# Performance work log

Measured on AMD Instinct MI355X. Metric: run time of the kernel, lower is better.

Reference implementation:

```python
import jax, jax.numpy as jnp
import numpy as np

N_NODES = 100000
N_EDGES = 1250000
D = 64
N_LAYERS = 4


def setup_inputs() -> dict:
    key = jax.random.key(0)
    ks = jax.random.split(key, 6)
    x = jax.random.normal(ks[0], (N_NODES, D), dtype=jnp.float32)
    edge_index = jax.random.randint(ks[1], (2, N_EDGES), 0, N_NODES, dtype=jnp.int64)
    s = 1.0 / np.sqrt(D)
    # PyG SAGEConv per layer: lin_l (applied to aggregated neighbors, with bias)
    # and lin_r (applied to self features, no bias). All layers are 64->64, so stack.
    Wl = jax.random.uniform(ks[2], (N_LAYERS, D, D), dtype=jnp.float32, minval=-s, maxval=s)
    bl = jax.random.uniform(ks[3], (N_LAYERS, D), dtype=jnp.float32, minval=-s, maxval=s)
    Wr = jax.random.uniform(ks[4], (N_LAYERS, D, D), dtype=jnp.float32, minval=-s, maxval=s)
    return {"x": x, "edge_index": edge_index, "Wl": Wl, "bl": bl, "Wr": Wr}


def reference(x, edge_index, Wl, bl, Wr):
    src = edge_index[0]  # message source: x_j
    dst = edge_index[1]  # aggregate at target node
    h = x
    for i in range(N_LAYERS):
        msg = h[src]  # [E, D] irregular gather
        agg = jax.ops.segment_max(msg, dst, num_segments=N_NODES)  # max-pool aggregation
        agg = jnp.where(jnp.isneginf(agg), 0.0, agg)  # empty segments -> 0 (PyG convention)
        h = jax.nn.relu(agg @ Wl[i] + bl[i] + h @ Wr[i])
    return h
```

## Files before the change

kernel.cpp:

```cpp
#include <hip/hip_runtime.h>
#include <hip/hip_fp16.h>
#include <stdint.h>

#define NN 100000
#define NE 1250000
#define DD 64
#define NL 4

#define NPART3 256
#define PSIZE3 391
#define TILE4 1024
#define NTB ((NE / 4 + TILE4 - 1) / TILE4)
#define SCANA_N (NPART3 * NTB)
#define SRCBITS 17

#define MB2 64
#define L2BLOCKS ((NN + MB2 - 1) / MB2)
#define APAD 136
#define CPADH 72
#define CPADF 68

typedef _Float16 half8 __attribute__((ext_vector_type(8)));
typedef _Float16 half2v __attribute__((ext_vector_type(2)));
typedef float floatx4 __attribute__((ext_vector_type(4)));
typedef int intx4 __attribute__((ext_vector_type(4)));

__device__ __forceinline__ unsigned f2h2(float a, float b) {
    __half2 h = __floats2half2_rn(a, b);
    return *reinterpret_cast<unsigned*>(&h);
}
__device__ __forceinline__ unsigned umax2(unsigned a, unsigned b) {
    half2v x = *reinterpret_cast<half2v*>(&a);
    half2v y = *reinterpret_cast<half2v*>(&b);
    half2v r = __builtin_elementwise_max(x, y);
    return *reinterpret_cast<unsigned*>(&r);
}

__global__ __launch_bounds__(256) void cast_kernel(const float* __restrict__ x,
                                                   __half* __restrict__ hh) {
    int i = blockIdx.x * 256 + threadIdx.x;
    float4 v = ((const float4*)x)[i];
    uint2 u;
    u.x = f2h2(v.x, v.y);
    u.y = f2h2(v.z, v.w);
    ((uint2*)hh)[i] = u;
}

__global__ __launch_bounds__(256) void countA_kernel(const int* __restrict__ dst,
                                                     int* __restrict__ blockcnt) {
    __shared__ int cnt[NPART3];
    int tid = threadIdx.x;
    cnt[tid] = 0;
    __syncthreads();
    int b = blockIdx.x;
    #pragma unroll
    for (int r = 0; r < 4; ++r) {
        int i4 = b * TILE4 + r * 256 + tid;
        if (i4 < NE / 4) {
            intx4 d = __builtin_nontemporal_load(&((const intx4*)dst)[i4]);
            atomicAdd(&cnt[(unsigned)d.x / PSIZE3], 1);
            atomicAdd(&cnt[(unsigned)d.y / PSIZE3], 1);
            atomicAdd(&cnt[(unsigned)d.z / PSIZE3], 1);
            atomicAdd(&cnt[(unsigned)d.w / PSIZE3], 1);
        }
    }
    __syncthreads();
    blockcnt[tid * NTB + b] = cnt[tid];
}

__global__ __launch_bounds__(512) void scanP1_kernel(int* __restrict__ blockcnt,
                                                     int* __restrict__ rowsum) {
    __shared__ int sm[512];
    int p = blockIdx.x;
    int tid = threadIdx.x;
    int v = (tid < NTB) ? blockcnt[p * NTB + tid] : 0;
    sm[tid] = v;
    __syncthreads();
    for (int off = 1; off < 512; off <<= 1) {
        int t = (tid >= off) ? sm[tid - off] : 0;
        __syncthreads();
        sm[tid] += t;
        __syncthreads();
    }
    if (tid < NTB) blockcnt[p * NTB + tid] = sm[tid] - v;
    if (tid == 511) rowsum[p] = sm[511];
}

__global__ __launch_bounds__(256) void scanP2_kernel(int* __restrict__ rowsum) {
    __shared__ int sm[256];
    int tid = threadIdx.x;
    int v = rowsum[tid];
    sm[tid] = v;
    __syncthreads();
    for (int off = 1; off < 256; off <<= 1) {
        int t = (tid >= off) ? sm[tid - off] : 0;
        __syncthreads();
        sm[tid] += t;
        __syncthreads();
    }
    rowsum[tid] = sm[tid] - v;
}

__global__ __launch_bounds__(256) void scatterA_kernel(const int* __restrict__ src,
                                                       const int* __restrict__ dst,
                                                       const int* __restrict__ blockcnt,
                                                       const int* __restrict__ rowoff,
                                                       int* __restrict__ ebufP) {
    __shared__ int cur[NPART3];
    int tid = threadIdx.x;
    int b = blockIdx.x;
    cur[tid] = rowoff[tid] + blockcnt[tid * NTB + b];
    __syncthreads();
    #pragma unroll
    for (int r = 0; r < 4; ++r) {
        int i4 = b * TILE4 + r * 256 + tid;
        if (i4 < NE / 4) {
            intx4 d = __builtin_nontemporal_load(&((const intx4*)dst)[i4]);
            intx4 s = __builtin_nontemporal_load(&((const intx4*)src)[i4]);
            int part, p;
            part = (unsigned)d.x / PSIZE3; p = atomicAdd(&cur[part], 1);
            ebufP[p] = ((d.x - part * PSIZE3) << SRCBITS) | s.x;
            part = (unsigned)d.y / PSIZE3; p = atomicAdd(&cur[part], 1);
            ebufP[p] = ((d.y - part * PSIZE3) << SRCBITS) | s.y;
            part = (unsigned)d.z / PSIZE3; p = atomicAdd(&cur[part], 1);
            ebufP[p] = ((d.z - part * PSIZE3) << SRCBITS) | s.z;
            part = (unsigned)d.w / PSIZE3; p = atomicAdd(&cur[part], 1);
            ebufP[p] = ((d.w - part * PSIZE3) << SRCBITS) | s.w;
        }
    }
}

__global__ __launch_bounds__(1024) void fillD_kernel(const int* __restrict__ ebufP,
                                                     const int* __restrict__ rowoff,
                                                     int* __restrict__ row_start,
                                                     int* __restrict__ csr) {
    __shared__ int cnt[PSIZE3];
    __shared__ int localstart[PSIZE3];
    __shared__ int partial[1024];
    int part = blockIdx.x;
    int tid = threadIdx.x;
    int nbase = part * PSIZE3;
    int base = rowoff[part];
    int hi = (part < NPART3 - 1) ? rowoff[part + 1] : NE;

    if (tid < PSIZE3) cnt[tid] = 0;
    __syncthreads();

    for (int i = base + tid; i < hi; i += 1024)
        atomicAdd(&cnt[(unsigned)ebufP[i] >> SRCBITS], 1);
    __syncthreads();

    int e0 = (tid < PSIZE3) ? cnt[tid] : 0;
    int s = e0;
    partial[tid] = s;
    __syncthreads();
    for (int off = 1; off < 1024; off <<= 1) {
        int v = (tid >= off) ? partial[tid - off] : 0;
        __syncthreads();
        partial[tid] += v;
        __syncthreads();
    }
    int run = partial[tid] - s;
    if (tid < PSIZE3) localstart[tid] = run;
    __syncthreads();

    int nmax = NN - nbase; if (nmax > PSIZE3) nmax = PSIZE3;
    if (tid < nmax) row_start[nbase + tid] = base + localstart[tid];
    if (part == NPART3 - 1 && tid == 0) row_start[NN] = NE;

    if (tid < PSIZE3) cnt[tid] = 0;
    __syncthreads();

    for (int i = base + tid; i < hi; i += 1024) {
        int p = ebufP[i];
        int dl = (unsigned)p >> SRCBITS;
        int local = atomicAdd(&cnt[dl], 1);
        csr[base + localstart[dl] + local] = p & ((1 << SRCBITS) - 1);
    }
}

__global__ __launch_bounds__(256) void agg_kernel(const __half* __restrict__ hh,
                                                  const int* __restrict__ row_start,
                                                  const int* __restrict__ csr,
                                                  __half* __restrict__ aggh) {
    int tid = threadIdx.x;
    int wv = tid >> 6;
    int lane = tid & 63;
    int g = lane >> 3;
    int c8 = (lane & 7) * 8;
    int n0 = blockIdx.x * 8 + wv * 2;
    int n1 = n0 + 1;
    int base0 = row_start[n0];
    int base1 = row_start[n1];
    int cnt0 = base1 - base0;
    int cnt1 = row_start[n1 + 1] - base1;
    int cl0 = cnt0 - 1;
    int cl1 = cnt1 - 1;

    int idx0 = 0, idx1 = 0;
    if (cnt0 > 0) idx0 = csr[base0 + ((lane <= cl0) ? lane : cl0)];
    if (cnt1 > 0) idx1 = csr[base1 + ((lane <= cl1) ? lane : cl1)];

    const uint4 NI4 = make_uint4(0xFC00FC00u, 0xFC00FC00u, 0xFC00FC00u, 0xFC00FC00u);
    uint4 acc0 = (cnt0 > 0) ? NI4 : make_uint4(0, 0, 0, 0);
    uint4 acc1 = (cnt1 > 0) ? NI4 : make_uint4(0, 0, 0, 0);

    int m0 = (cnt0 < 64) ? cnt0 : 64;
    int m1 = (cnt1 < 64) ? cnt1 : 64;
    int kmax = (m0 > m1) ? m0 : m1;

    for (int k = 0; k < kmax; k += 16) {
        int ka = k + g;
        int kb = k + g + 8;
        int s00 = 0, s01 = 0, s10 = 0, s11 = 0;
        if (cnt0 > 0) {
            s00 = __shfl(idx0, (ka <= cl0) ? ka : cl0, 64);
            s01 = __shfl(idx0, (kb <= cl0) ? kb : cl0, 64);
        }
        if (cnt1 > 0) {
            s10 = __shfl(idx1, (ka <= cl1) ? ka : cl1, 64);
            s11 = __shfl(idx1, (kb <= cl1) ? kb : cl1, 64);
        }
        if (ka < m0) {
            uint4 u = *(const uint4*)&hh[(size_t)s00 * DD + c8];
            acc0.x = umax2(acc0.x, u.x); acc0.y = umax2(acc0.y, u.y);
            acc0.z = umax2(acc0.z, u.z); acc0.w = umax2(acc0.w, u.w);
        }
        if (ka < m1) {
            uint4 u = *(const uint4*)&hh[(size_t)s10 * DD + c8];
            acc1.x = umax2(acc1.x, u.x); acc1.y = umax2(acc1.y, u.y);
            acc1.z = umax2(acc1.z, u.z); acc1.w = umax2(acc1.w, u.w);
        }
        if (kb < m0) {
            uint4 u = *(const uint4*)&hh[(size_t)s01 * DD + c8];
            acc0.x = umax2(acc0.x, u.x); acc0.y = umax2(acc0.y, u.y);
            acc0.z = umax2(acc0.z, u.z); acc0.w = umax2(acc0.w, u.w);
        }
        if (kb < m1) {
            uint4 u = *(const uint4*)&hh[(size_t)s11 * DD + c8];
            acc1.x = umax2(acc1.x, u.x); acc1.y = umax2(acc1.y, u.y);
            acc1.z = umax2(acc1.z, u.z); acc1.w = umax2(acc1.w, u.w);
        }
    }
    for (int k = 64 + g; k < cnt0; k += 8) {
        int s = csr[base0 + k];
        uint4 u = *(const uint4*)&hh[(size_t)s * DD + c8];
        acc0.x = umax2(acc0.x, u.x); acc0.y = umax2(acc0.y, u.y);
        acc0.z = umax2(acc0.z, u.z); acc0.w = umax2(acc0.w, u.w);
    }
    for (int k = 64 + g; k < cnt1; k += 8) {
        int s = csr[base1 + k];
        uint4 u = *(const uint4*)&hh[(size_t)s * DD + c8];
        acc1.x = umax2(acc1.x, u.x); acc1.y = umax2(acc1.y, u.y);
        acc1.z = umax2(acc1.z, u.z); acc1.w = umax2(acc1.w, u.w);
    }

    #pragma unroll
    for (int off = 8; off <= 32; off <<= 1) {
        acc0.x = umax2(acc0.x, (unsigned)__shfl_xor((int)acc0.x, off, 64));
        acc0.y = umax2(acc0.y, (unsigned)__shfl_xor((int)acc0.y, off, 64));
        acc0.z = umax2(acc0.z, (unsigned)__shfl_xor((int)acc0.z, off, 64));
        acc0.w = umax2(acc0.w, (unsigned)__shfl_xor((int)acc0.w, off, 64));
        acc1.x = umax2(acc1.x, (unsigned)__shfl_xor((int)acc1.x, off, 64));
        acc1.y = umax2(acc1.y, (unsigned)__shfl_xor((int)acc1.y, off, 64));
        acc1.z = umax2(acc1.z, (unsigned)__shfl_xor((int)acc1.z, off, 64));
        acc1.w = umax2(acc1.w, (unsigned)__shfl_xor((int)acc1.w, off, 64));
    }
    if (lane < 8) {
        *(uint4*)&aggh[(size_t)n0 * DD + c8] = acc0;
        *(uint4*)&aggh[(size_t)n1 * DD + c8] = acc1;
    }
}

__global__ __launch_bounds__(256, 4) void layer_mfma_kernel(
        const __half* __restrict__ aggh,
        __half* __restrict__ hh,
        float* __restrict__ hout,
        const float* __restrict__ Wl,
        const float* __restrict__ bl,
        const float* __restrict__ Wr,
        int last) {
    __shared__ char smem[2 * MB2 * APAD * 2];
    _Float16* a_s  = (_Float16*)smem;
    _Float16* bt_s = (_Float16*)(smem + MB2 * APAD * 2);

    int tid = threadIdx.x;
    int lane = tid & 63;
    int w = tid >> 6;
    int node0 = blockIdx.x * MB2;

    #pragma unroll
    for (int i = 0; i < 4; ++i) {
        int idx = i * 256 + tid;
        int r = idx >> 4;
        int c4 = idx & 15;
        int node = node0 + r; if (node > NN - 1) node = NN - 1;
        const __half* srcp = (c4 < 8) ? (aggh + (size_t)node * DD + c4 * 8)
                                      : (hh + (size_t)node * DD + (c4 - 8) * 8);
        uint4 v = *(const uint4*)srcp;
        *(uint4*)&a_s[r * APAD + c4 * 8] = v;
    }
    {
        int n = tid & 63;
        int kb = tid >> 6;
        #pragma unroll
        for (int kk = 0; kk < 32; ++kk) {
            int k = kb * 32 + kk;
            float wv = (k < 64) ? Wl[k * DD + n] : Wr[(k - 64) * DD + n];
            bt_s[n * APAD + k] = (_Float16)wv;
        }
    }
    __syncthreads();

    floatx4 acc[4];
    #pragma unroll
    for (int nt = 0; nt < 4; ++nt) acc[nt] = (floatx4){0.f, 0.f, 0.f, 0.f};
    int m = lane & 15;
    int q = lane >> 4;

    #pragma unroll
    for (int ks = 0; ks < 4; ++ks) {
        half8 af = *(half8*)&a_s[(w * 16 + m) * APAD + q * 8 + ks * 32];
        #pragma unroll
        for (int nt = 0; nt < 4; ++nt) {
            half8 bf = *(half8*)&bt_s[(nt * 16 + m) * APAD + q * 8 + ks * 32];
            acc[nt] = __builtin_amdgcn_mfma_f32_16x16x32_f16(af, bf, acc[nt], 0, 0, 0);
        }
    }
    __syncthreads();

    _Float16* ch = (_Float16*)smem;
    float*    cf = (float*)(smem + MB2 * CPADH * 2);

    #pragma unroll
    for (int nt = 0; nt < 4; ++nt) {
        int col = nt * 16 + m;
        float b = bl[col];
        #pragma unroll
        for (int r = 0; r < 4; ++r) {
            int rowl = w * 16 + q * 4 + r;
            float o = fmaxf(acc[nt][r] + b, 0.0f);
            if (last) cf[rowl * CPADF + col] = o;
            else      ch[rowl * CPADH + col] = (_Float16)o;
        }
    }
    __syncthreads();

    if (!last) {
        #pragma unroll
        for (int i = 0; i < 2; ++i) {
            int idx = i * 256 + tid;
            int r = idx >> 3;
            int c4 = idx & 7;
            int node = node0 + r;
            if (node < NN) {
                uint4 v = *(uint4*)&ch[r * CPADH + c4 * 8];
                *(uint4*)&hh[(size_t)node * DD + c4 * 8] = v;
            }
        }
    } else {
        #pragma unroll
        for (int i = 0; i < 4; ++i) {
            int idx = i * 256 + tid;
            int r = idx >> 4;
            int c4 = idx & 15;
            int node = node0 + r;
            if (node < NN) {
                float4 v = *(float4*)&cf[r * CPADF + c4 * 4];
                *(float4*)&hout[(size_t)node * DD + c4 * 4] = v;
            }
        }
    }
}

extern "C" void kernel_launch(void* const* d_in, const int* in_sizes, int n_in,
                              void* d_out, int out_size, void* d_ws, size_t ws_size,
                              hipStream_t stream) {
    const float* x  = (const float*)d_in[0];
    const int*   ei = (const int*)d_in[1];
    const float* Wl = (const float*)d_in[2];
    const float* bl = (const float*)d_in[3];
    const float* Wr = (const float*)d_in[4];
    float* h = (float*)d_out;

    const int* src = ei;
    const int* dst = ei + NE;

    char* ws = (char*)d_ws;
    __half* aggh     = (__half*)ws;  ws += (size_t)NN * DD * sizeof(__half);
    __half* hh       = (__half*)ws;  ws += (size_t)NN * DD * sizeof(__half);
    int* row_start   = (int*)ws;     ws += (size_t)(NN + 16) * sizeof(int);
    int* blockcnt    = (int*)ws;     ws += (size_t)(SCANA_N + 16) * sizeof(int);
    int* rowsum      = (int*)ws;     ws += (size_t)(NPART3 + 16) * sizeof(int);
    int* csr         = (int*)ws;

    int* ebufP = (int*)aggh;

    cast_kernel<<<(NN * DD / 4) / 256, 256, 0, stream>>>(x, hh);

    countA_kernel<<<NTB, 256, 0, stream>>>(dst, blockcnt);
    scanP1_kernel<<<NPART3, 512, 0, stream>>>(blockcnt, rowsum);
    scanP2_kernel<<<1, 256, 0, stream>>>(rowsum);
    scatterA_kernel<<<NTB, 256, 0, stream>>>(src, dst, blockcnt, rowsum, ebufP);
    fillD_kernel<<<NPART3, 1024, 0, stream>>>(ebufP, rowsum, row_start, csr);

    for (int l = 0; l < NL; ++l) {
        agg_kernel<<<NN / 8, 256, 0, stream>>>(hh, row_start, csr, aggh);
        layer_mfma_kernel<<<L2BLOCKS, 256, 0, stream>>>(
            aggh, hh, h, Wl + (size_t)l * DD * DD, bl + (size_t)l * DD, Wr + (size_t)l * DD * DD,
            (l == NL - 1) ? 1 : 0);
    }
}
```

Before: 282.4 us.

## Split feature table into four column slabs for cache-local gather aggregation

Stores the fp16 node features and aggregates as four column slabs of 16 halves each (slab-major), and runs the max-aggregation with a 2D grid where blockIdx.y selects the slab. Each slab is 3.2 MB, so a pass over one slab's random gathers is meant to stay resident in L2/LLC instead of thrashing the full 12.8 MB table. The agg kernel now handles 4 nodes per wave with 16 lanes each, and uses nontemporal loads for the CSR. In exchange the CSR and row_start are read four times, and the cast and MFMA kernels take strided slab addressing.

```diff
diff --git a/kernel.cpp b/kernel.cpp
--- a/kernel.cpp
+++ b/kernel.cpp
@@ -37,13 +37,18 @@
 }
 
 __global__ __launch_bounds__(256) void cast_kernel(const float* __restrict__ x,
-                                                   __half* __restrict__ hh) {
+                                                   __half* __restrict__ hh4) {
     int i = blockIdx.x * 256 + threadIdx.x;
     float4 v = ((const float4*)x)[i];
     uint2 u;
     u.x = f2h2(v.x, v.y);
     u.y = f2h2(v.z, v.w);
-    ((uint2*)hh)[i] = u;
+    int j = i * 4;
+    int n = j >> 6;
+    int col = j & 63;
+    int s = col >> 4;
+    int c = col & 15;
+    ((uint2*)hh4)[((size_t)s * NN + n) * 4 + (c >> 2)] = u;
 }
 
 __global__ __launch_bounds__(256) void countA_kernel(const int* __restrict__ dst,
@@ -179,102 +184,68 @@
     }
 }
 
-__global__ __launch_bounds__(256) void agg_kernel(const __half* __restrict__ hh,
+__global__ __launch_bounds__(256) void agg_kernel(const __half* __restrict__ hh4,
                                                   const int* __restrict__ row_start,
                                                   const int* __restrict__ csr,
-                                                  __half* __restrict__ aggh) {
+                                                  __half* __restrict__ agg4) {
     int tid = threadIdx.x;
     int wv = tid >> 6;
     int lane = tid & 63;
-    int g = lane >> 3;
-    int c8 = (lane & 7) * 8;
-    int n0 = blockIdx.x * 8 + wv * 2;
-    int n1 = n0 + 1;
-    int base0 = row_start[n0];
-    int base1 = row_start[n1];
-    int cnt0 = base1 - base0;
-    int cnt1 = row_start[n1 + 1] - base1;
-    int cl0 = cnt0 - 1;
-    int cl1 = cnt1 - 1;
-
-    int idx0 = 0, idx1 = 0;
-    if (cnt0 > 0) idx0 = csr[base0 + ((lane <= cl0) ? lane : cl0)];
-    if (cnt1 > 0) idx1 = csr[base1 + ((lane <= cl1) ? lane : cl1)];
+    int nq = lane >> 4;
+    int l16 = lane & 15;
+    int sl = l16 >> 1;
+    int sub = lane & 1;
+    int s = blockIdx.y;
+    int n = blockIdx.x * 16 + wv * 4 + nq;
+
+    int base = row_start[n];
+    int cnt  = row_start[n + 1] - base;
+    int cl = cnt - 1;
+
+    int idx16 = 0;
+    if (cnt > 0) idx16 = __builtin_nontemporal_load(&csr[base + ((l16 <= cl) ? l16 : cl)]);
+
+    const __half* tab = hh4 + (size_t)s * NN * 16;
 
     const uint4 NI4 = make_uint4(0xFC00FC00u, 0xFC00FC00u, 0xFC00FC00u, 0xFC00FC00u);
-    uint4 acc0 = (cnt0 > 0) ? NI4 : make_uint4(0, 0, 0, 0);
-    uint4 acc1 = (cnt1 > 0) ? NI4 : make_uint4(0, 0, 0, 0);
-
-    int m0 = (cnt0 < 64) ? cnt0 : 64;
-    int m1 = (cnt1 < 64) ? cnt1 : 64;
-    int kmax = (m0 > m1) ? m0 : m1;
-
-    for (int k = 0; k < kmax; k += 16) {
-        int ka = k + g;
-        int kb = k + g + 8;
-        int s00 = 0, s01 = 0, s10 = 0, s11 = 0;
-        if (cnt0 > 0) {
-            s00 = __shfl(idx0, (ka <= cl0) ? ka : cl0, 64);
-            s01 = __shfl(idx0, (kb <= cl0) ? kb : cl0, 64);
-        }
-        if (cnt1 > 0) {
-            s10 = __shfl(idx1, (ka <= cl1) ? ka : cl1, 64);
-            s11 = __shfl(idx1, (kb <= cl1) ? kb : cl1, 64);
-        }
-        if (ka < m0) {
-            uint4 u = *(const uint4*)&hh[(size_t)s00 * DD + c8];
-            acc0.x = umax2(acc0.x, u.x); acc0.y = umax2(acc0.y, u.y);
-            acc0.z = umax2(acc0.z, u.z); acc0.w = umax2(acc0.w, u.w);
-        }
-        if (ka < m1) {
-            uint4 u = *(const uint4*)&hh[(size_t)s10 * DD + c8];
-            acc1.x = umax2(acc1.x, u.x); acc1.y = umax2(acc1.y, u.y);
-            acc1.z = umax2(acc1.z, u.z); acc1.w = umax2(acc1.w, u.w);
-        }
-        if (kb < m0) {
-            uint4 u = *(const uint4*)&hh[(size_t)s01 * DD + c8];
-            acc0.x = umax2(acc0.x, u.x); acc0.y = umax2(acc0.y, u.y);
-            acc0.z = umax2(acc0.z, u.z); acc0.w = umax2(acc0.w, u.w);
-        }
-        if (kb < m1) {
-            uint4 u = *(const uint4*)&hh[(size_t)s11 * DD + c8];
-            acc1.x = umax2(acc1.x, u.x); acc1.y = umax2(acc1.y, u.y);
-            acc1.z = umax2(acc1.z, u.z); acc1.w = umax2(acc1.w, u.w);
-        }
-    }
-    for (int k = 64 + g; k < cnt0; k += 8) {
-        int s = csr[base0 + k];
-        uint4 u = *(const uint4*)&hh[(size_t)s * DD + c8];
-        acc0.x = umax2(acc0.x, u.x); acc0.y = umax2(acc0.y, u.y);
-        acc0.z = umax2(acc0.z, u.z); acc0.w = umax2(acc0.w, u.w);
-    }
-    for (int k = 64 + g; k < cnt1; k += 8) {
-        int s = csr[base1 + k];
-        uint4 u = *(const uint4*)&hh[(size_t)s * DD + c8];
-        acc1.x = umax2(acc1.x, u.x); acc1.y = umax2(acc1.y, u.y);
-        acc1.z = umax2(acc1.z, u.z); acc1.w = umax2(acc1.w, u.w);
-    }
-
-    #pragma unroll
-    for (int off = 8; off <= 32; off <<= 1) {
-        acc0.x = umax2(acc0.x, (unsigned)__shfl_xor((int)acc0.x, off, 64));
-        acc0.y = umax2(acc0.y, (unsigned)__shfl_xor((int)acc0.y, off, 64));
-        acc0.z = umax2(acc0.z, (unsigned)__shfl_xor((int)acc0.z, off, 64));
-        acc0.w = umax2(acc0.w, (unsigned)__shfl_xor((int)acc0.w, off, 64));
-        acc1.x = umax2(acc1.x, (unsigned)__shfl_xor((int)acc1.x, off, 64));
-        acc1.y = umax2(acc1.y, (unsigned)__shfl_xor((int)acc1.y, off, 64));
-        acc1.z = umax2(acc1.z, (unsigned)__shfl_xor((int)acc1.z, off, 64));
-        acc1.w = umax2(acc1.w, (unsigned)__shfl_xor((int)acc1.w, off, 64));
-    }
-    if (lane < 8) {
-        *(uint4*)&aggh[(size_t)n0 * DD + c8] = acc0;
-        *(uint4*)&aggh[(size_t)n1 * DD + c8] = acc1;
+    uint4 acc = (cnt > 0) ? NI4 : make_uint4(0, 0, 0, 0);
+
+    int km = cnt;
+    km = max(km, __shfl_xor(km, 16, 64));
+    km = max(km, __shfl_xor(km, 32, 64));
+
+    for (int k = 0; k < km; k += 8) {
+        int ka = k + sl;
+        int srcv;
+        if (k < 16) {
+            int cka = (ka <= cl) ? ka : cl;
+            if (cka < 0) cka = 0;
+            srcv = __shfl(idx16, (nq << 4) + cka, 64);
+        } else {
+            srcv = (ka < cnt) ? __builtin_nontemporal_load(&csr[base + ka]) : 0;
+        }
+        if (ka < cnt) {
+            uint4 u = *(const uint4*)&tab[(size_t)srcv * 16 + sub * 8];
+            acc.x = umax2(acc.x, u.x); acc.y = umax2(acc.y, u.y);
+            acc.z = umax2(acc.z, u.z); acc.w = umax2(acc.w, u.w);
+        }
+    }
+
+    #pragma unroll
+    for (int off = 2; off <= 8; off <<= 1) {
+        acc.x = umax2(acc.x, (unsigned)__shfl_xor((int)acc.x, off, 64));
+        acc.y = umax2(acc.y, (unsigned)__shfl_xor((int)acc.y, off, 64));
+        acc.z = umax2(acc.z, (unsigned)__shfl_xor((int)acc.z, off, 64));
+        acc.w = umax2(acc.w, (unsigned)__shfl_xor((int)acc.w, off, 64));
+    }
+    if (l16 < 2) {
+        *(uint4*)&agg4[((size_t)s * NN + n) * 16 + sub * 8] = acc;
     }
 }
 
 __global__ __launch_bounds__(256, 4) void layer_mfma_kernel(
-        const __half* __restrict__ aggh,
-        __half* __restrict__ hh,
+        const __half* __restrict__ agg4,
+        __half* __restrict__ hh4,
         float* __restrict__ hout,
         const float* __restrict__ Wl,
         const float* __restrict__ bl,
@@ -295,8 +266,12 @@
         int r = idx >> 4;
         int c4 = idx & 15;
         int node = node0 + r; if (node > NN - 1) node = NN - 1;
-        const __half* srcp = (c4 < 8) ? (aggh + (size_t)node * DD + c4 * 8)
-                                      : (hh + (size_t)node * DD + (c4 - 8) * 8);
+        const __half* srcp;
+        if (c4 < 8) srcp = agg4 + ((size_t)(c4 >> 1) * NN + node) * 16 + (c4 & 1) * 8;
+        else {
+            int cc = c4 - 8;
+            srcp = hh4 + ((size_t)(cc >> 1) * NN + node) * 16 + (cc & 1) * 8;
+        }
         uint4 v = *(const uint4*)srcp;
         *(uint4*)&a_s[r * APAD + c4 * 8] = v;
     }
@@ -355,7 +330,7 @@
             int node = node0 + r;
             if (node < NN) {
                 uint4 v = *(uint4*)&ch[r * CPADH + c4 * 8];
-                *(uint4*)&hh[(size_t)node * DD + c4 * 8] = v;
+                *(uint4*)&hh4[((size_t)(c4 >> 1) * NN + node) * 16 + (c4 & 1) * 8] = v;
             }
         }
     } else {
@@ -387,16 +362,16 @@
     const int* dst = ei + NE;
 
     char* ws = (char*)d_ws;
-    __half* aggh     = (__half*)ws;  ws += (size_t)NN * DD * sizeof(__half);
-    __half* hh       = (__half*)ws;  ws += (size_t)NN * DD * sizeof(__half);
+    __half* agg4     = (__half*)ws;  ws += (size_t)NN * DD * sizeof(__half);
+    __half* hh4      = (__half*)ws;  ws += (size_t)NN * DD * sizeof(__half);
     int* row_start   = (int*)ws;     ws += (size_t)(NN + 16) * sizeof(int);
     int* blockcnt    = (int*)ws;     ws += (size_t)(SCANA_N + 16) * sizeof(int);
     int* rowsum      = (int*)ws;     ws += (size_t)(NPART3 + 16) * sizeof(int);
     int* csr         = (int*)ws;
 
-    int* ebufP = (int*)aggh;
-
-    cast_kernel<<<(NN * DD / 4) / 256, 256, 0, stream>>>(x, hh);
+    int* ebufP = (int*)agg4;
+
+    cast_kernel<<<(NN * DD / 4) / 256, 256, 0, stream>>>(x, hh4);
 
     countA_kernel<<<NTB, 256, 0, stream>>>(dst, blockcnt);
     scanP1_kernel<<<NPART3, 512, 0, stream>>>(blockcnt, rowsum);
@@ -405,9 +380,9 @@
     fillD_kernel<<<NPART3, 1024, 0, stream>>>(ebufP, rowsum, row_start, csr);
 
     for (int l = 0; l < NL; ++l) {
-        agg_kernel<<<NN / 8, 256, 0, stream>>>(hh, row_start, csr, aggh);
+        agg_kernel<<<dim3(NN / 16, 4), 256, 0, stream>>>(hh4, row_start, csr, agg4);
         layer_mfma_kernel<<<L2BLOCKS, 256, 0, stream>>>(
-            aggh, hh, h, Wl + (size_t)l * DD * DD, bl + (size_t)l * DD, Wr + (size_t)l * DD * DD,
+            agg4, hh4, h, Wl + (size_t)l * DD * DD, bl + (size_t)l * DD, Wr + (size_t)l * DD * DD,
             (l == NL - 1) ? 1 : 0);
     }
 }
```

After: 358.6 us. 1.27x slower.
